# Performance work log

Measured on AMD Instinct MI355X. Metric: run time of the kernel, lower is better.

The kernel has to match this reference:

```python
import jax, jax.numpy as jnp
import numpy as np

U, I, NB = 200000, 100000, 50000
D = 64
NUM_LAYERS = 2
TEMP = 0.25      # conf['c_temps']
ALPHA = 0.5      # conf['alpha']
E_UI, E_UB, E_BI = 4_000_000, 2_000_000, 2_000_000
BT = 4096


def _segsum(vals, idx, gathered, n):
    # SpMM: out[idx] += vals * gathered   (COO sparse matmul)
    return jax.ops.segment_sum(vals[:, None] * gathered, idx, num_segments=n)


def _propagate(xa, xb, rows, cols, vals, layers):
    # LightGCN-style propagation over the symmetric bipartite block matrix
    # [[0, A], [A^T, 0]] with layer averaging.
    acc_a, acc_b = xa, xb
    for _ in range(layers):
        na = _segsum(vals, rows, xb[cols], xa.shape[0])
        nb = _segsum(vals, cols, xa[rows], xb.shape[0])
        xa, xb = na, nb
        acc_a = acc_a + xa
        acc_b = acc_b + xb
    inv = 1.0 / (layers + 1)
    return acc_a * inv, acc_b * inv


def _info_nce(a, b, temp):
    a = a * jax.lax.rsqrt(jnp.sum(a * a, -1, keepdims=True) + 1e-8)
    b = b * jax.lax.rsqrt(jnp.sum(b * b, -1, keepdims=True) + 1e-8)
    logits = (a @ b.T) / temp                      # [BT, BT]
    return jnp.mean(jax.nn.logsumexp(logits, axis=-1) - jnp.diagonal(logits))


def setup_inputs() -> dict:
    key = jax.random.key(0)
    ks = jax.random.split(key, 20)
    sc = 1.0 / np.sqrt(D)
    f32 = jnp.float32
    return {
        "users_feat": jax.random.normal(ks[0], (U, D), f32) * sc,
        "bundles_feat": jax.random.normal(ks[1], (NB, D), f32) * sc,
        "items_feat": jax.random.normal(ks[2], (I, D), f32) * sc,
        "L1_w": jax.random.normal(ks[3], (3, 3), f32) * 0.5,
        "L1_b": jnp.zeros((3,), f32),
        "L2_w": jax.random.normal(ks[4], (3, 3), f32) * 0.5,
        "L2_b": jnp.zeros((3,), f32),
        "L3_w": jax.random.normal(ks[5], (1, 3), f32) * 0.5,
        "L3_b": jnp.zeros((1,), f32),
        "ui_val": jax.random.uniform(ks[6], (E_UI,), f32, 0.0, 0.05),
        "ub_val": jax.random.uniform(ks[7], (E_UB,), f32, 0.0, 0.05),
        "bi_val": jax.random.uniform(ks[8], (E_BI,), f32, 0.0, 0.05),
        "ui_row": jax.random.randint(ks[9], (E_UI,), 0, U, jnp.int32),
        "ui_col": jax.random.randint(ks[10], (E_UI,), 0, I, jnp.int32),
        "ub_row": jax.random.randint(ks[11], (E_UB,), 0, U, jnp.int32),
        "ub_col": jax.random.randint(ks[12], (E_UB,), 0, NB, jnp.int32),
        "bi_row": jax.random.randint(ks[13], (E_BI,), 0, NB, jnp.int32),
        "bi_col": jax.random.randint(ks[14], (E_BI,), 0, I, jnp.int32),
        "users_idx": jax.random.randint(ks[15], (BT,), 0, U, jnp.int32),
        "bundles_idx": jax.random.randint(ks[16], (BT, 2), 0, NB, jnp.int32),
    }


def reference(users_feat, bundles_feat, items_feat, L1_w, L1_b, L2_w, L2_b,
              L3_w, L3_b, ui_val, ub_val, bi_val, ui_row, ui_col, ub_row,
              ub_col, bi_row, bi_col, users_idx, bundles_idx):
    # View 1: item-level main graph (u-i Laplacian propagation), bundle rep
    # aggregated from item embeddings via the row-normalized b-i graph.
    u1, i1 = _propagate(users_feat, items_feat, ui_row, ui_col, ui_val, NUM_LAYERS)
    b1 = _segsum(bi_val, bi_row, i1[bi_col], NB)
    # View 2: bundle-level main graph (u-b Laplacian propagation).
    u2, b2 = _propagate(users_feat, bundles_feat, ub_row, ub_col, ub_val, NUM_LAYERS)
    # View 3: sub views, one-hop row-normalized aggregation of raw item embs.
    u3 = _segsum(ui_val, ui_row, items_feat[ui_col], U)
    b3 = _segsum(bi_val, bi_row, items_feat[bi_col], NB)

    ue = jnp.stack([u1[users_idx], u2[users_idx], u3[users_idx]], axis=-1)      # [BT,D,3]
    be = jnp.stack([b1[bundles_idx], b2[bundles_idx], b3[bundles_idx]], axis=-1)  # [BT,2,D,3]
    s = jnp.einsum('bdv,bpdv->bpv', ue, be)                                      # [BT,2,3]

    # L1/L2/L3 view-fusion MLP (3 -> 3 -> 3 -> 1)
    h = jnp.tanh(s @ L1_w.T + L1_b)
    h = jnp.tanh(h @ L2_w.T + L2_b)
    pred = (h @ L3_w.T + L3_b)[..., 0]                                           # [BT,2]

    # BPR: -log sigmoid(pos - neg) == softplus(neg - pos)
    bpr = jnp.mean(jax.nn.softplus(-(pred[:, 0] - pred[:, 1])))
    cl = (_info_nce(u1[users_idx], u2[users_idx], TEMP)
          + _info_nce(b1[bundles_idx[:, 0]], b2[bundles_idx[:, 0]], TEMP))
    return bpr + ALPHA * cl
```

## Files before the change

### kernel.cpp

```cpp
#include <hip/hip_runtime.h>
#include <math.h>

#define DD 64
#define SCAN_TPB 256
#define SCAN_EPT 8
#define SCAN_EPB (SCAN_TPB * SCAN_EPT)
#define NCHUNK 8

__device__ __forceinline__ float bf2f(unsigned short u) {
    return __uint_as_float(((unsigned)u) << 16);
}
__device__ __forceinline__ unsigned short f2bf(float x) {
    unsigned b = __float_as_uint(x);
    unsigned r = (b + 0x7fffu + ((b >> 16) & 1u)) >> 16;
    return (unsigned short)r;
}


__global__ void hist_chunked_kernel(int* __restrict__ cnt, const int* __restrict__ tgt,
                                    int E, int n) {
    int myc = blockIdx.x & (NCHUNK - 1);
    int sub = blockIdx.x >> 3;
    int nsub = gridDim.x >> 3;
    int start = sub * blockDim.x + threadIdx.x;
    int stride = nsub * blockDim.x;
    for (int e = start; e < E; e += stride) {
        int t_ = tgt[e];
        int c = (int)(((long long)t_ * NCHUNK) / n);
        if (c == myc) atomicAdd(&cnt[t_], 1);
    }
}

__global__ void scatter_pairs_chunked(int2* __restrict__ pairs, int* __restrict__ cursor,
                                      const int* __restrict__ tgt, const int* __restrict__ src,
                                      const float* __restrict__ val, int E, int n) {
    int myc = blockIdx.x & (NCHUNK - 1);
    int sub = blockIdx.x >> 3;
    int nsub = gridDim.x >> 3;
    int start = sub * blockDim.x + threadIdx.x;
    int stride = nsub * blockDim.x;
    for (int e = start; e < E; e += stride) {
        int t_ = tgt[e];
        int c = (int)(((long long)t_ * NCHUNK) / n);
        if (c == myc) {
            int2 pr;
            pr.x = src[e];
            pr.y = __float_as_int(val[e]);
            int p = atomicAdd(&cursor[t_], 1);
            pairs[p] = pr;
        }
    }
}

__global__ void mark_kernel(int* __restrict__ mark, const int* __restrict__ idx, int n) {
    int g = blockIdx.x * blockDim.x + threadIdx.x;
    if (g < n) mark[idx[g]] = 1;
}

__global__ void hist_marked_kernel(int* __restrict__ cnt, const int* __restrict__ tgt,
                                   const int* __restrict__ mark, int E) {
    int g = blockIdx.x * blockDim.x + threadIdx.x;
    int stride = gridDim.x * blockDim.x;
    for (int e = g; e < E; e += stride) {
        int t_ = tgt[e];
        if (mark[t_]) atomicAdd(&cnt[t_], 1);
    }
}

__global__ void scatter_marked_kernel(int2* __restrict__ pairs, int* __restrict__ cursor,
                                      const int* __restrict__ tgt, const int* __restrict__ src,
                                      const float* __restrict__ val,
                                      const int* __restrict__ mark, int E) {
    int g = blockIdx.x * blockDim.x + threadIdx.x;
    int stride = gridDim.x * blockDim.x;
    for (int e = g; e < E; e += stride) {
        int t_ = tgt[e];
        if (mark[t_]) {
            int2 pr;
            pr.x = src[e];
            pr.y = __float_as_int(val[e]);
            int p = atomicAdd(&cursor[t_], 1);
            pairs[p] = pr;
        }
    }
}

__global__ void scan_pass1(int* __restrict__ blocksum, const int* __restrict__ cnt, int n) {
    int base = blockIdx.x * SCAN_EPB + threadIdx.x * SCAN_EPT;
    int s = 0;
#pragma unroll
    for (int k = 0; k < SCAN_EPT; ++k) {
        int i = base + k;
        if (i < n) s += cnt[i];
    }
#pragma unroll
    for (int o = 32; o >= 1; o >>= 1) s += __shfl_xor(s, o);
    __shared__ int ws_[4];
    if ((threadIdx.x & 63) == 0) ws_[threadIdx.x >> 6] = s;
    __syncthreads();
    if (threadIdx.x == 0) blocksum[blockIdx.x] = ws_[0] + ws_[1] + ws_[2] + ws_[3];
}

__global__ void scan_pass2(int* __restrict__ blocksum, int nb, int* __restrict__ ptr_n) {
    __shared__ int sh[1024];
    int t = threadIdx.x;
    int v = (t < nb) ? blocksum[t] : 0;
    sh[t] = v;
    __syncthreads();
    for (int o = 1; o < 1024; o <<= 1) {
        int x = (t >= o) ? sh[t - o] : 0;
        __syncthreads();
        sh[t] += x;
        __syncthreads();
    }
    if (t < nb) blocksum[t] = sh[t] - v;
    if (t == nb - 1) ptr_n[0] = sh[t];
}

__global__ void scan_pass3(int* __restrict__ ptr, int* __restrict__ cursor,
                           const int* __restrict__ cnt, const int* __restrict__ blockoff,
                           int n) {
    int base = blockIdx.x * SCAN_EPB + threadIdx.x * SCAN_EPT;
    int vals[SCAN_EPT];
    int s = 0;
#pragma unroll
    for (int k = 0; k < SCAN_EPT; ++k) {
        int i = base + k;
        int c = (i < n) ? cnt[i] : 0;
        vals[k] = s;
        s += c;
    }
    int incl = s;
#pragma unroll
    for (int o = 1; o < 64; o <<= 1) {
        int x = __shfl_up(incl, o);
        if ((threadIdx.x & 63) >= o) incl += x;
    }
    __shared__ int wtot[4];
    if ((threadIdx.x & 63) == 63) wtot[threadIdx.x >> 6] = incl;
    __syncthreads();
    int woff = 0;
    int wv = threadIdx.x >> 6;
    for (int k = 0; k < 4; ++k)
        if (k < wv) woff += wtot[k];
    int texcl = incl - s + woff + blockoff[blockIdx.x];
#pragma unroll
    for (int k = 0; k < SCAN_EPT; ++k) {
        int i = base + k;
        if (i < n) {
            int p = texcl + vals[k];
            ptr[i] = p;
            cursor[i] = p;
        }
    }
}

__global__ void spmm_kernel(const float* __restrict__ inf, const unsigned short* __restrict__ inb,
                            const int2* __restrict__ pairs, const int* __restrict__ ptr,
                            int nrows, const int* __restrict__ rowidx,
                            float* __restrict__ out, unsigned short* __restrict__ outb,
                            const float* __restrict__ add1,
                            const float* __restrict__ add2f,
                            const unsigned short* __restrict__ add2b,
                            float scale1,
                            const float* __restrict__ in2f, const unsigned short* __restrict__ in2b,
                            float* __restrict__ out2, const float* __restrict__ addB,
                            float f, float scale2) {
    int w = (int)(((unsigned)blockIdx.x * blockDim.x + threadIdx.x) >> 6);
    int lane = threadIdx.x & 63;
    if (w >= nrows) return;
    int r = rowidx ? rowidx[w] : w;
    int p = ptr[r];
    int end = ptr[r + 1];
    size_t outoff = (size_t)w * DD + lane;
    size_t nodeoff = (size_t)r * DD + lane;
    float acc = 0.f, acc2 = 0.f;
    const bool dual = (in2f != nullptr) || (in2b != nullptr);
    for (; p + 8 <= end; p += 8) {
        int ss[8];
        float vv[8];
#pragma unroll
        for (int k = 0; k < 8; ++k) {
            int2 pr = pairs[p + k];
            ss[k] = __builtin_amdgcn_readfirstlane(pr.x);
            vv[k] = __int_as_float(__builtin_amdgcn_readfirstlane(pr.y));
        }
        if (inb) {
#pragma unroll
            for (int k = 0; k < 8; ++k) acc += vv[k] * bf2f(inb[(size_t)ss[k] * DD + lane]);
        } else {
#pragma unroll
            for (int k = 0; k < 8; ++k) acc += vv[k] * inf[(size_t)ss[k] * DD + lane];
        }
        if (dual) {
            if (in2b) {
#pragma unroll
                for (int k = 0; k < 8; ++k) acc2 += vv[k] * bf2f(in2b[(size_t)ss[k] * DD + lane]);
            } else {
#pragma unroll
                for (int k = 0; k < 8; ++k) acc2 += vv[k] * in2f[(size_t)ss[k] * DD + lane];
            }
        }
    }
    for (; p < end; ++p) {
        int2 pr = pairs[p];
        int s = __builtin_amdgcn_readfirstlane(pr.x);
        float v = __int_as_float(__builtin_amdgcn_readfirstlane(pr.y));
        acc += v * (inb ? bf2f(inb[(size_t)s * DD + lane]) : inf[(size_t)s * DD + lane]);
        if (dual)
            acc2 += v * (in2b ? bf2f(in2b[(size_t)s * DD + lane]) : in2f[(size_t)s * DD + lane]);
    }
    float rr = acc;
    if (add1) rr += add1[nodeoff];
    if (add2f) rr += add2f[nodeoff];
    if (add2b) rr += bf2f(add2b[nodeoff]);
    rr *= scale1;
    if (out) out[outoff] = rr;
    if (outb) outb[outoff] = f2bf(rr);
    if (dual) {
        float r2 = acc2 + f * acc;
        if (addB) r2 += addB[nodeoff];
        out2[outoff] = r2 * scale2;
    }
}


__global__ void f2bf_kernel(unsigned short* __restrict__ o, const float* __restrict__ i,
                            long long n4) {
    long long g = (long long)blockIdx.x * blockDim.x + threadIdx.x;
    long long stride = (long long)gridDim.x * blockDim.x;
    for (long long t = g; t < n4; t += stride) {
        float4 v = ((const float4*)i)[t];
        ushort4 u;
        u.x = f2bf(v.x); u.y = f2bf(v.y); u.z = f2bf(v.z); u.w = f2bf(v.w);
        ((ushort4*)o)[t] = u;
    }
}

__global__ void gather_rows_bf16_kernel(float* __restrict__ raw,
                                        const unsigned short* __restrict__ src,
                                        const int* __restrict__ idx, int nrows) {
    int g = blockIdx.x * blockDim.x + threadIdx.x;
    if (g >= nrows * DD) return;
    int r = g >> 6;
    raw[g] = bf2f(src[(size_t)idx[r] * DD + (g & 63)]);
}

__global__ void norm_rows_kernel(float* __restrict__ nrm, const float* __restrict__ src,
                                 int nrows, int rstride) {
    int r = blockIdx.x;
    if (r >= nrows) return;
    int d = threadIdx.x;
    float v = src[(size_t)r * rstride * DD + d];
    float ss = v * v;
#pragma unroll
    for (int o = 32; o >= 1; o >>= 1) ss += __shfl_xor(ss, o);
    nrm[(size_t)r * DD + d] = v * rsqrtf(ss + 1e-8f);
}

__global__ void transpose64_kernel(float* __restrict__ out, const float* __restrict__ in,
                                   int n) {
    __shared__ float T[64][65];
    int b0 = blockIdx.x * 64;
    int t = threadIdx.x;
#pragma unroll
    for (int k = 0; k < 4; ++k) {
        int f = k * 1024 + t * 4;
        int r = f >> 6, c = f & 63;
        float4 v = *(const float4*)(in + (size_t)(b0 + r) * 64 + c);
        T[r][c] = v.x; T[r][c + 1] = v.y; T[r][c + 2] = v.z; T[r][c + 3] = v.w;
    }
    __syncthreads();
#pragma unroll
    for (int k = 0; k < 4; ++k) {
        int f = k * 1024 + t * 4;
        int d = f >> 6, c = f & 63;
        float4 v;
        v.x = T[c][d]; v.y = T[c + 1][d]; v.z = T[c + 2][d]; v.w = T[c + 3][d];
        *(float4*)(out + (size_t)d * n + b0 + c) = v;
    }
}

__global__ void batch_pred_kernel(const float* __restrict__ u1b, const float* __restrict__ u2b,
                                  const float* __restrict__ u3b,
                                  const float* __restrict__ b1b, const float* __restrict__ b2b,
                                  const float* __restrict__ b3b,
                                  const float* __restrict__ W1, const float* __restrict__ c1,
                                  const float* __restrict__ W2, const float* __restrict__ c2,
                                  const float* __restrict__ W3, const float* __restrict__ c3,
                                  float* __restrict__ acc, int nb) {
    int b = blockIdx.x;
    if (b >= nb) return;
    int d = threadIdx.x;
    float ud1 = u1b[(size_t)b * DD + d];
    float ud2 = u2b[(size_t)b * DD + d];
    float ud3 = u3b[(size_t)b * DD + d];
    float pred[2];
#pragma unroll
    for (int p = 0; p < 2; ++p) {
        size_t r = (size_t)(b * 2 + p) * DD + d;
        float s0 = ud1 * b1b[r];
        float s1 = ud2 * b2b[r];
        float s2 = ud3 * b3b[r];
#pragma unroll
        for (int o = 32; o >= 1; o >>= 1) {
            s0 += __shfl_xor(s0, o);
            s1 += __shfl_xor(s1, o);
            s2 += __shfl_xor(s2, o);
        }
        float t0 = tanhf(s0 * W1[0] + s1 * W1[1] + s2 * W1[2] + c1[0]);
        float t1 = tanhf(s0 * W1[3] + s1 * W1[4] + s2 * W1[5] + c1[1]);
        float t2 = tanhf(s0 * W1[6] + s1 * W1[7] + s2 * W1[8] + c1[2]);
        float g0 = tanhf(t0 * W2[0] + t1 * W2[1] + t2 * W2[2] + c2[0]);
        float g1 = tanhf(t0 * W2[3] + t1 * W2[4] + t2 * W2[5] + c2[1]);
        float g2 = tanhf(t0 * W2[6] + t1 * W2[7] + t2 * W2[8] + c2[2]);
        pred[p] = g0 * W3[0] + g1 * W3[1] + g2 * W3[2] + c3[0];
    }
    if (d == 0) {
        float x = pred[1] - pred[0];
        float sp = (x > 20.0f) ? x : log1pf(expf(x));
        unsafeAtomicAdd(acc, sp);
    }
}

__global__ void nce_part_kernel(const float* __restrict__ A, const float* __restrict__ Bt,
                                float* __restrict__ pm, float* __restrict__ ps,
                                float* __restrict__ pd, int n, float invtemp) {
    int wv = threadIdx.x >> 6;
    int lane = threadIdx.x & 63;
    int row = blockIdx.x;
    float4 a4[16];
    const float4* Ap = (const float4*)(A + (size_t)row * DD);
#pragma unroll
    for (int q = 0; q < 16; ++q) a4[q] = Ap[q];
    int quarter = n >> 2;
    int c0 = wv * quarter;
    float m = -1e30f, ssum = 0.0f, diag = 0.0f;
    int ntile = quarter >> 8;
    for (int t = 0; t < ntile; ++t) {
        int j0 = c0 + (t << 8) + (lane << 2);
        float dx = 0.f, dy = 0.f, dz = 0.f, dw = 0.f;
#pragma unroll
        for (int q = 0; q < 16; ++q) {
            float4 a = a4[q];
            float4 r0 = *(const float4*)(Bt + (size_t)(4 * q + 0) * n + j0);
            float4 r1 = *(const float4*)(Bt + (size_t)(4 * q + 1) * n + j0);
            float4 r2 = *(const float4*)(Bt + (size_t)(4 * q + 2) * n + j0);
            float4 r3 = *(const float4*)(Bt + (size_t)(4 * q + 3) * n + j0);
            dx += a.x * r0.x + a.y * r1.x + a.z * r2.x + a.w * r3.x;
            dy += a.x * r0.y + a.y * r1.y + a.z * r2.y + a.w * r3.y;
            dz += a.x * r0.z + a.y * r1.z + a.z * r2.z + a.w * r3.z;
            dw += a.x * r0.w + a.y * r1.w + a.z * r2.w + a.w * r3.w;
        }
        float lg[4] = {dx * invtemp, dy * invtemp, dz * invtemp, dw * invtemp};
#pragma unroll
        for (int k = 0; k < 4; ++k) {
            if (j0 + k == row) diag = lg[k];
            float mn = fmaxf(m, lg[k]);
            ssum = ssum * __expf(m - mn) + __expf(lg[k] - mn);
            m = mn;
        }
    }
#pragma unroll
    for (int o = 32; o >= 1; o >>= 1) {
        float m2 = __shfl_xor(m, o);
        float s2 = __shfl_xor(ssum, o);
        float d2 = __shfl_xor(diag, o);
        float mn = fmaxf(m, m2);
        ssum = ssum * __expf(m - mn) + s2 * __expf(m2 - mn);
        m = mn;
        diag += d2;
    }
    if (lane == 0) {
        pm[row * 4 + wv] = m;
        ps[row * 4 + wv] = ssum;
        pd[row * 4 + wv] = diag;
    }
}

__global__ void nce_merge_kernel(const float* __restrict__ pm, const float* __restrict__ ps,
                                 const float* __restrict__ pd, float* __restrict__ acc,
                                 int nrows) {
    int r = blockIdx.x * blockDim.x + threadIdx.x;
    float v = 0.0f;
    if (r < nrows) {
        float m = -1e30f, s = 0.f, d = 0.f;
#pragma unroll
        for (int q = 0; q < 4; ++q) {
            float mq = pm[r * 4 + q], sq = ps[r * 4 + q];
            d += pd[r * 4 + q];
            float mn = fmaxf(m, mq);
            s = s * __expf(m - mn) + sq * __expf(mq - mn);
            m = mn;
        }
        v = m + logf(s) - d;
    }
#pragma unroll
    for (int o = 32; o >= 1; o >>= 1) v += __shfl_xor(v, o);
    if ((threadIdx.x & 63) == 0) unsafeAtomicAdd(acc, v);
}

__global__ void final_kernel(const float* __restrict__ acc, float* __restrict__ out,
                             float invn, float alpha) {
    out[0] = acc[0] * invn + alpha * invn * (acc[1] + acc[2]);
}


extern "C" void kernel_launch(void* const* d_in, const int* in_sizes, int n_in,
                              void* d_out, int out_size, void* d_ws, size_t ws_size,
                              hipStream_t stream) {
    const float* users_feat   = (const float*)d_in[0];
    const float* bundles_feat = (const float*)d_in[1];
    const float* items_feat   = (const float*)d_in[2];
    const float* W1 = (const float*)d_in[3];
    const float* c1 = (const float*)d_in[4];
    const float* W2 = (const float*)d_in[5];
    const float* c2 = (const float*)d_in[6];
    const float* W3 = (const float*)d_in[7];
    const float* c3 = (const float*)d_in[8];
    const float* ui_val = (const float*)d_in[9];
    const float* ub_val = (const float*)d_in[10];
    const float* bi_val = (const float*)d_in[11];
    const int* ui_row = (const int*)d_in[12];
    const int* ui_col = (const int*)d_in[13];
    const int* ub_row = (const int*)d_in[14];
    const int* ub_col = (const int*)d_in[15];
    const int* bi_row = (const int*)d_in[16];
    const int* bi_col = (const int*)d_in[17];
    const int* uidx = (const int*)d_in[18];
    const int* bidx = (const int*)d_in[19];

    const int U  = in_sizes[0] / DD;
    const int NB = in_sizes[1] / DD;
    const int I  = in_sizes[2] / DD;
    const int Eui = in_sizes[9];
    const int Eub = in_sizes[10];
    const int Ebi = in_sizes[11];
    const int BT = in_sizes[18];

    const size_t U64  = (size_t)U * DD;
    const size_t I64  = (size_t)I * DD;
    const size_t NB64 = (size_t)NB * DD;
    const size_t BT64 = (size_t)BT * DD;

    float* w = (float*)d_ws;
    size_t o = 0;
    float* RA  = w + o; o += I64;
    float* RB  = w + o; o += I64;
    float* u3b = w + o; o += BT64;
    float* u1b = w + o; o += BT64;
    float* u2b = w + o; o += BT64;
    float* b1b = w + o; o += 2 * BT64;
    float* b2b = w + o; o += 2 * BT64;
    float* b3b = w + o; o += 2 * BT64;
    float* A1  = w + o; o += BT64;
    float* A2  = w + o; o += BT64;
    float* B1n = w + o; o += BT64;
    float* B2n = w + o; o += BT64;
    float* pm  = w + o; o += (size_t)BT * 4;
    float* ps  = w + o; o += (size_t)BT * 4;
    float* pd  = w + o; o += (size_t)BT * 4;
    float* acc = w + o; o += 16;

    unsigned short* Ubf = (unsigned short*)(w + o); o += (U64 + 1) / 2;
    unsigned short* Ibf = (unsigned short*)(w + o); o += (I64 + 1) / 2;
    unsigned short* Bbf = (unsigned short*)(w + o); o += (NB64 + 1) / 2;
    unsigned short* Xbf = (unsigned short*)(w + o); o += (U64 + 1) / 2;

    int nmax = U; if (I > nmax) nmax = I; if (NB > nmax) nmax = NB;
    int emax = Eui; if (Eub > emax) emax = Eub; if (Ebi > emax) emax = Ebi;
    int* ib = (int*)(w + o);
    size_t io_ = 0;
    int* cnt  = ib + io_; io_ += (size_t)nmax + 1;
    int* bsum = ib + io_; io_ += 1025;
    int* mark = ib + io_; io_ += (size_t)NB + 1;
    int* ptrA = ib + io_; io_ += (size_t)nmax + 1;
    int* ptrB = ib + io_; io_ += (size_t)nmax + 1;
    io_ = (io_ + 3) & ~(size_t)3;
    int2* pairsA = (int2*)(ib + io_); io_ += (size_t)emax * 2;
    int2* pairsB = (int2*)(ib + io_); io_ += (size_t)emax * 2;

    float* A2t = (float*)pairsA;
    float* B2t = A2t + BT64;

    auto build = [&](int2* pairs, int* ptr_, const int* tgt, const int* src,
                     const float* val, int n, int E) {
        hipMemsetAsync(cnt, 0, ((size_t)n + 1) * sizeof(int), stream);
        hist_chunked_kernel<<<8192, 256, 0, stream>>>(cnt, tgt, E, n);
        int nb_ = (n + SCAN_EPB - 1) / SCAN_EPB;
        scan_pass1<<<nb_, SCAN_TPB, 0, stream>>>(bsum, cnt, n);
        scan_pass2<<<1, 1024, 0, stream>>>(bsum, nb_, ptr_ + n);
        scan_pass3<<<nb_, SCAN_TPB, 0, stream>>>(ptr_, cnt, cnt, bsum, n);
        scatter_pairs_chunked<<<8192, 256, 0, stream>>>(pairs, cnt, tgt, src, val, E, n);
    };
    auto spmm = [&](const float* inf, const unsigned short* inb,
                    const int2* pairs, const int* ptr_, int nrows, const int* rowidx,
                    float* out, unsigned short* outb,
                    const float* add1, const float* add2f, const unsigned short* add2b,
                    float scale1,
                    const float* in2f, const unsigned short* in2b,
                    float* out2, const float* addB, float f, float scale2) {
        int blocks = (nrows + 3) / 4;
        spmm_kernel<<<blocks, 256, 0, stream>>>(inf, inb, pairs, ptr_, nrows, rowidx,
                                                out, outb, add1, add2f, add2b, scale1,
                                                in2f, in2b, out2, addB, f, scale2);
    };
    const float k3 = 1.0f / 3.0f;
    const float* NF = nullptr;
    const unsigned short* NB16 = nullptr;
    const int* NI = nullptr;

    f2bf_kernel<<<2048, 256, 0, stream>>>(Ubf, users_feat, (long long)(U64 / 4));
    f2bf_kernel<<<1024, 256, 0, stream>>>(Ibf, items_feat, (long long)(I64 / 4));
    f2bf_kernel<<<512, 256, 0, stream>>>(Bbf, bundles_feat, (long long)(NB64 / 4));

    build(pairsA, ptrA, ui_row, ui_col, ui_val, U, Eui);
    spmm(NF, Ibf, pairsA, ptrA, U, NI,
         nullptr, Xbf, NF, NF, NB16, 1.f, NF, NB16, nullptr, NF, 0.f, 1.f);
    gather_rows_bf16_kernel<<<(BT * DD + 255) / 256, 256, 0, stream>>>(u3b, Xbf, uidx, BT);
    build(pairsB, ptrB, ui_col, ui_row, ui_val, I, Eui);
    spmm(NF, Ubf, pairsB, ptrB, I, NI,
         RA, nullptr, NF, NF, NB16, 1.f,
         NF, Xbf, RB, items_feat, 1.f, k3);
    spmm(RA, NB16, pairsA, ptrA, BT, uidx,
         u1b, nullptr, users_feat, NF, Xbf, k3, NF, NB16, nullptr, NF, 0.f, 1.f);
    norm_rows_kernel<<<BT, 64, 0, stream>>>(A1, u1b, BT, 1);

    hipMemsetAsync(mark, 0, ((size_t)NB + 1) * sizeof(int), stream);
    mark_kernel<<<(2 * BT + 255) / 256, 256, 0, stream>>>(mark, bidx, 2 * BT);
    hipMemsetAsync(cnt, 0, ((size_t)NB + 1) * sizeof(int), stream);
    {
        int gb = (Ebi + 255) / 256; if (gb > 4096) gb = 4096;
        hist_marked_kernel<<<gb, 256, 0, stream>>>(cnt, bi_row, mark, Ebi);
        int nb_ = (NB + SCAN_EPB - 1) / SCAN_EPB;
        scan_pass1<<<nb_, SCAN_TPB, 0, stream>>>(bsum, cnt, NB);
        scan_pass2<<<1, 1024, 0, stream>>>(bsum, nb_, ptrA + NB);
        scan_pass3<<<nb_, SCAN_TPB, 0, stream>>>(ptrA, cnt, cnt, bsum, NB);
        scatter_marked_kernel<<<gb, 256, 0, stream>>>(pairsA, cnt, bi_row, bi_col,
                                                      bi_val, mark, Ebi);
    }
    spmm(RB, NB16, pairsA, ptrA, 2 * BT, bidx,
         b1b, nullptr, NF, NF, NB16, 1.f,
         NF, Ibf, b3b, NF, 0.f, 1.f);
    norm_rows_kernel<<<BT, 64, 0, stream>>>(B1n, b1b, BT, 2);

    build(pairsA, ptrA, ub_row, ub_col, ub_val, U, Eub);
    spmm(NF, Bbf, pairsA, ptrA, U, NI,
         nullptr, Xbf, NF, NF, NB16, 1.f, NF, NB16, nullptr, NF, 0.f, 1.f);
    build(pairsB, ptrB, ub_col, ub_row, ub_val, NB, Eub);
    spmm(NF, Ubf, pairsB, ptrB, NB, NI,
         RA, nullptr, NF, NF, NB16, 1.f, NF, NB16, nullptr, NF, 0.f, 1.f);
    spmm(RA, NB16, pairsA, ptrA, BT, uidx,
         u2b, nullptr, users_feat, NF, Xbf, k3, NF, NB16, nullptr, NF, 0.f, 1.f);
    norm_rows_kernel<<<BT, 64, 0, stream>>>(A2, u2b, BT, 1);
    spmm(NF, Xbf, pairsB, ptrB, 2 * BT, bidx,
         b2b, nullptr, bundles_feat, RA, NB16, k3, NF, NB16, nullptr, NF, 0.f, 1.f);
    norm_rows_kernel<<<BT, 64, 0, stream>>>(B2n, b2b, BT, 2);

    transpose64_kernel<<<BT / 64, 256, 0, stream>>>(A2t, A2, BT);
    transpose64_kernel<<<BT / 64, 256, 0, stream>>>(B2t, B2n, BT);

    hipMemsetAsync(acc, 0, 4 * sizeof(float), stream);

    batch_pred_kernel<<<BT, 64, 0, stream>>>(u1b, u2b, u3b, b1b, b2b, b3b,
                                             W1, c1, W2, c2, W3, c3, acc, BT);

    nce_part_kernel<<<BT, 256, 0, stream>>>(A1, A2t, pm, ps, pd, BT, 4.0f);
    nce_merge_kernel<<<(BT + 255) / 256, 256, 0, stream>>>(pm, ps, pd, acc + 1, BT);
    nce_part_kernel<<<BT, 256, 0, stream>>>(B1n, B2t, pm, ps, pd, BT, 4.0f);
    nce_merge_kernel<<<(BT + 255) / 256, 256, 0, stream>>>(pm, ps, pd, acc + 2, BT);

    final_kernel<<<1, 1, 0, stream>>>(acc, (float*)d_out, 1.0f / (float)BT, 0.5f);
}
```

Measured before the change: 2.330 ms.

## Compute InfoNCE logits with bf16 MFMA and fuse row normalization into SpMM

Replaces the scalar fp32 InfoNCE dot-product kernel, its merge kernel and the transposes with one MFMA-based kernel. It takes bf16 normalized rows and handles both contrastive terms in a single launch, doing the online logsumexp per 16-row tile. Row L2 normalization moves into the SpMM epilogue, which writes bf16 directly and removes the separate normalize kernels. The cost is bf16 precision in the logits. The InfoNCE stage is only a small part of a runtime dominated by the sparse builds and SpMMs.

```diff
diff --git a/kernel.cpp b/kernel.cpp
--- a/kernel.cpp
+++ b/kernel.cpp
@@ -6,6 +6,9 @@
 #define SCAN_EPT 8
 #define SCAN_EPB (SCAN_TPB * SCAN_EPT)
 #define NCHUNK 8
+
+typedef short bf16x8 __attribute__((ext_vector_type(8)));
+typedef float f32x4 __attribute__((ext_vector_type(4)));
 
 __device__ __forceinline__ float bf2f(unsigned short u) {
     return __uint_as_float(((unsigned)u) << 16);
@@ -165,7 +168,8 @@
                             float scale1,
                             const float* __restrict__ in2f, const unsigned short* __restrict__ in2b,
                             float* __restrict__ out2, const float* __restrict__ addB,
-                            float f, float scale2) {
+                            float f, float scale2,
+                            unsigned short* __restrict__ nrmOut, int nrmEvery) {
     int w = (int)(((unsigned)blockIdx.x * blockDim.x + threadIdx.x) >> 6);
     int lane = threadIdx.x & 63;
     if (w >= nrows) return;
@@ -222,6 +226,12 @@
         if (addB) r2 += addB[nodeoff];
         out2[outoff] = r2 * scale2;
     }
+    if (nrmOut && (nrmEvery == 1 || (w & 1) == 0)) {
+        float sq = rr * rr;
+#pragma unroll
+        for (int o = 32; o >= 1; o >>= 1) sq += __shfl_xor(sq, o);
+        nrmOut[(size_t)(w / nrmEvery) * DD + lane] = f2bf(rr * rsqrtf(sq + 1e-8f));
+    }
 }
 
 
@@ -244,41 +254,6 @@
     if (g >= nrows * DD) return;
     int r = g >> 6;
     raw[g] = bf2f(src[(size_t)idx[r] * DD + (g & 63)]);
-}
-
-__global__ void norm_rows_kernel(float* __restrict__ nrm, const float* __restrict__ src,
-                                 int nrows, int rstride) {
-    int r = blockIdx.x;
-    if (r >= nrows) return;
-    int d = threadIdx.x;
-    float v = src[(size_t)r * rstride * DD + d];
-    float ss = v * v;
-#pragma unroll
-    for (int o = 32; o >= 1; o >>= 1) ss += __shfl_xor(ss, o);
-    nrm[(size_t)r * DD + d] = v * rsqrtf(ss + 1e-8f);
-}
-
-__global__ void transpose64_kernel(float* __restrict__ out, const float* __restrict__ in,
-                                   int n) {
-    __shared__ float T[64][65];
-    int b0 = blockIdx.x * 64;
-    int t = threadIdx.x;
-#pragma unroll
-    for (int k = 0; k < 4; ++k) {
-        int f = k * 1024 + t * 4;
-        int r = f >> 6, c = f & 63;
-        float4 v = *(const float4*)(in + (size_t)(b0 + r) * 64 + c);
-        T[r][c] = v.x; T[r][c + 1] = v.y; T[r][c + 2] = v.z; T[r][c + 3] = v.w;
-    }
-    __syncthreads();
-#pragma unroll
-    for (int k = 0; k < 4; ++k) {
-        int f = k * 1024 + t * 4;
-        int d = f >> 6, c = f & 63;
-        float4 v;
-        v.x = T[c][d]; v.y = T[c + 1][d]; v.z = T[c + 2][d]; v.w = T[c + 3][d];
-        *(float4*)(out + (size_t)d * n + b0 + c) = v;
-    }
 }
 
 __global__ void batch_pred_kernel(const float* __restrict__ u1b, const float* __restrict__ u2b,
@@ -323,81 +298,91 @@
     }
 }
 
-__global__ void nce_part_kernel(const float* __restrict__ A, const float* __restrict__ Bt,
-                                float* __restrict__ pm, float* __restrict__ ps,
-                                float* __restrict__ pd, int n, float invtemp) {
-    int wv = threadIdx.x >> 6;
-    int lane = threadIdx.x & 63;
-    int row = blockIdx.x;
-    float4 a4[16];
-    const float4* Ap = (const float4*)(A + (size_t)row * DD);
-#pragma unroll
-    for (int q = 0; q < 16; ++q) a4[q] = Ap[q];
-    int quarter = n >> 2;
-    int c0 = wv * quarter;
-    float m = -1e30f, ssum = 0.0f, diag = 0.0f;
-    int ntile = quarter >> 8;
+__global__ void nce_mfma_kernel(const unsigned short* __restrict__ A1,
+                                const unsigned short* __restrict__ B1, float* __restrict__ acc1,
+                                const unsigned short* __restrict__ A2,
+                                const unsigned short* __restrict__ B2, float* __restrict__ acc2,
+                                int n, float invtemp) {
+    int nbv = n >> 4;
+    const unsigned short* A;
+    const unsigned short* B;
+    float* accp;
+    int blk = blockIdx.x;
+    if (blk < nbv) { A = A1; B = B1; accp = acc1; }
+    else           { blk -= nbv; A = A2; B = B2; accp = acc2; }
+    int row0 = blk << 4;
+    int wv = threadIdx.x >> 6, lane = threadIdx.x & 63;
+    int li = lane & 15, lq = lane >> 4;
+
+    const bf16x8* Ap = (const bf16x8*)(A + (size_t)(row0 + li) * DD + lq * 8);
+    bf16x8 af0 = Ap[0];
+    bf16x8 af1 = Ap[4];
+
+    int qcols = n >> 2;
+    int c0 = wv * qcols;
+    int ntile = qcols >> 4;
+    float m[4] = {-1e30f, -1e30f, -1e30f, -1e30f};
+    float sm[4] = {0.f, 0.f, 0.f, 0.f};
+    float dg[4] = {0.f, 0.f, 0.f, 0.f};
     for (int t = 0; t < ntile; ++t) {
-        int j0 = c0 + (t << 8) + (lane << 2);
-        float dx = 0.f, dy = 0.f, dz = 0.f, dw = 0.f;
-#pragma unroll
-        for (int q = 0; q < 16; ++q) {
-            float4 a = a4[q];
-            float4 r0 = *(const float4*)(Bt + (size_t)(4 * q + 0) * n + j0);
-            float4 r1 = *(const float4*)(Bt + (size_t)(4 * q + 1) * n + j0);
-            float4 r2 = *(const float4*)(Bt + (size_t)(4 * q + 2) * n + j0);
-            float4 r3 = *(const float4*)(Bt + (size_t)(4 * q + 3) * n + j0);
-            dx += a.x * r0.x + a.y * r1.x + a.z * r2.x + a.w * r3.x;
-            dy += a.x * r0.y + a.y * r1.y + a.z * r2.y + a.w * r3.y;
-            dz += a.x * r0.z + a.y * r1.z + a.z * r2.z + a.w * r3.z;
-            dw += a.x * r0.w + a.y * r1.w + a.z * r2.w + a.w * r3.w;
-        }
-        float lg[4] = {dx * invtemp, dy * invtemp, dz * invtemp, dw * invtemp};
-#pragma unroll
-        for (int k = 0; k < 4; ++k) {
-            if (j0 + k == row) diag = lg[k];
-            float mn = fmaxf(m, lg[k]);
-            ssum = ssum * __expf(m - mn) + __expf(lg[k] - mn);
-            m = mn;
-        }
-    }
-#pragma unroll
-    for (int o = 32; o >= 1; o >>= 1) {
-        float m2 = __shfl_xor(m, o);
-        float s2 = __shfl_xor(ssum, o);
-        float d2 = __shfl_xor(diag, o);
-        float mn = fmaxf(m, m2);
-        ssum = ssum * __expf(m - mn) + s2 * __expf(m2 - mn);
-        m = mn;
-        diag += d2;
-    }
-    if (lane == 0) {
-        pm[row * 4 + wv] = m;
-        ps[row * 4 + wv] = ssum;
-        pd[row * 4 + wv] = diag;
-    }
-}
-
-__global__ void nce_merge_kernel(const float* __restrict__ pm, const float* __restrict__ ps,
-                                 const float* __restrict__ pd, float* __restrict__ acc,
-                                 int nrows) {
-    int r = blockIdx.x * blockDim.x + threadIdx.x;
-    float v = 0.0f;
-    if (r < nrows) {
-        float m = -1e30f, s = 0.f, d = 0.f;
+        int colbase = c0 + (t << 4);
+        const bf16x8* Bp = (const bf16x8*)(B + (size_t)(colbase + li) * DD + lq * 8);
+        bf16x8 bf0 = Bp[0];
+        bf16x8 bf1 = Bp[4];
+        f32x4 z = {0.f, 0.f, 0.f, 0.f};
+        f32x4 s = __builtin_amdgcn_mfma_f32_16x16x32_bf16(af0, bf0, z, 0, 0, 0);
+        s = __builtin_amdgcn_mfma_f32_16x16x32_bf16(af1, bf1, s, 0, 0, 0);
+        int col = colbase + li;
+#pragma unroll
+        for (int r = 0; r < 4; ++r) {
+            float l = s[r] * invtemp;
+            int row = row0 + (lq << 2) + r;
+            if (col == row) dg[r] = l;
+            float mn = fmaxf(m[r], l);
+            sm[r] = sm[r] * __expf(m[r] - mn) + __expf(l - mn);
+            m[r] = mn;
+        }
+    }
+#pragma unroll
+    for (int r = 0; r < 4; ++r) {
+        float mm = m[r], ss = sm[r], dd = dg[r];
+#pragma unroll
+        for (int o = 1; o <= 8; o <<= 1) {
+            float m2 = __shfl_xor(mm, o);
+            float s2 = __shfl_xor(ss, o);
+            float d2 = __shfl_xor(dd, o);
+            float mn = fmaxf(mm, m2);
+            ss = ss * __expf(mm - mn) + s2 * __expf(m2 - mn);
+            mm = mn;
+            dd += d2;
+        }
+        m[r] = mm; sm[r] = ss; dg[r] = dd;
+    }
+    __shared__ float pM[4][16], pS[4][16], pD[4][16];
+    if (li == 0) {
+#pragma unroll
+        for (int r = 0; r < 4; ++r) {
+            pM[wv][(lq << 2) + r] = m[r];
+            pS[wv][(lq << 2) + r] = sm[r];
+            pD[wv][(lq << 2) + r] = dg[r];
+        }
+    }
+    __syncthreads();
+    if (wv == 0 && lane < 16) {
+        float mm = -1e30f, ss = 0.f, dd = 0.f;
 #pragma unroll
         for (int q = 0; q < 4; ++q) {
-            float mq = pm[r * 4 + q], sq = ps[r * 4 + q];
-            d += pd[r * 4 + q];
-            float mn = fmaxf(m, mq);
-            s = s * __expf(m - mn) + sq * __expf(mq - mn);
-            m = mn;
-        }
-        v = m + logf(s) - d;
-    }
-#pragma unroll
-    for (int o = 32; o >= 1; o >>= 1) v += __shfl_xor(v, o);
-    if ((threadIdx.x & 63) == 0) unsafeAtomicAdd(acc, v);
+            float mq = pM[q][lane], sq = pS[q][lane];
+            dd += pD[q][lane];
+            float mn = fmaxf(mm, mq);
+            ss = ss * __expf(mm - mn) + sq * __expf(mq - mn);
+            mm = mn;
+        }
+        float v = mm + logf(ss) - dd;
+#pragma unroll
+        for (int o = 1; o <= 8; o <<= 1) v += __shfl_xor(v, o);
+        if (lane == 0) unsafeAtomicAdd(accp, v);
+    }
 }
 
 __global__ void final_kernel(const float* __restrict__ acc, float* __restrict__ out,
@@ -453,13 +438,10 @@
     float* b1b = w + o; o += 2 * BT64;
     float* b2b = w + o; o += 2 * BT64;
     float* b3b = w + o; o += 2 * BT64;
-    float* A1  = w + o; o += BT64;
-    float* A2  = w + o; o += BT64;
-    float* B1n = w + o; o += BT64;
-    float* B2n = w + o; o += BT64;
-    float* pm  = w + o; o += (size_t)BT * 4;
-    float* ps  = w + o; o += (size_t)BT * 4;
-    float* pd  = w + o; o += (size_t)BT * 4;
+    unsigned short* A1  = (unsigned short*)(w + o); o += BT64 / 2;
+    unsigned short* A2  = (unsigned short*)(w + o); o += BT64 / 2;
+    unsigned short* B1n = (unsigned short*)(w + o); o += BT64 / 2;
+    unsigned short* B2n = (unsigned short*)(w + o); o += BT64 / 2;
     float* acc = w + o; o += 16;
 
     unsigned short* Ubf = (unsigned short*)(w + o); o += (U64 + 1) / 2;
@@ -479,9 +461,6 @@
     io_ = (io_ + 3) & ~(size_t)3;
     int2* pairsA = (int2*)(ib + io_); io_ += (size_t)emax * 2;
     int2* pairsB = (int2*)(ib + io_); io_ += (size_t)emax * 2;
-
-    float* A2t = (float*)pairsA;
-    float* B2t = A2t + BT64;
 
     auto build = [&](int2* pairs, int* ptr_, const int* tgt, const int* src,
                      const float* val, int n, int E) {
@@ -499,11 +478,13 @@
                     const float* add1, const float* add2f, const unsigned short* add2b,
                     float scale1,
                     const float* in2f, const unsigned short* in2b,
-                    float* out2, const float* addB, float f, float scale2) {
+                    float* out2, const float* addB, float f, float scale2,
+                    unsigned short* nrmOut, int nrmEvery) {
         int blocks = (nrows + 3) / 4;
         spmm_kernel<<<blocks, 256, 0, stream>>>(inf, inb, pairs, ptr_, nrows, rowidx,
                                                 out, outb, add1, add2f, add2b, scale1,
-                                                in2f, in2b, out2, addB, f, scale2);
+                                                in2f, in2b, out2, addB, f, scale2,
+                                                nrmOut, nrmEvery);
     };
     const float k3 = 1.0f / 3.0f;
     const float* NF = nullptr;
@@ -516,16 +497,17 @@
 
     build(pairsA, ptrA, ui_row, ui_col, ui_val, U, Eui);
     spmm(NF, Ibf, pairsA, ptrA, U, NI,
-         nullptr, Xbf, NF, NF, NB16, 1.f, NF, NB16, nullptr, NF, 0.f, 1.f);
+         nullptr, Xbf, NF, NF, NB16, 1.f, NF, NB16, nullptr, NF, 0.f, 1.f,
+         nullptr, 1);
     gather_rows_bf16_kernel<<<(BT * DD + 255) / 256, 256, 0, stream>>>(u3b, Xbf, uidx, BT);
     build(pairsB, ptrB, ui_col, ui_row, ui_val, I, Eui);
     spmm(NF, Ubf, pairsB, ptrB, I, NI,
          RA, nullptr, NF, NF, NB16, 1.f,
-         NF, Xbf, RB, items_feat, 1.f, k3);
+         NF, Xbf, RB, items_feat, 1.f, k3,
+         nullptr, 1);
     spmm(RA, NB16, pairsA, ptrA, BT, uidx,
-         u1b, nullptr, users_feat, NF, Xbf, k3, NF, NB16, nullptr, NF, 0.f, 1.f);
-    norm_rows_kernel<<<BT, 64, 0, stream>>>(A1, u1b, BT, 1);
-
+         u1b, nullptr, users_feat, NF, Xbf, k3, NF, NB16, nullptr, NF, 0.f, 1.f,
+         A1, 1);
     hipMemsetAsync(mark, 0, ((size_t)NB + 1) * sizeof(int), stream);
     mark_kernel<<<(2 * BT + 255) / 256, 256, 0, stream>>>(mark, bidx, 2 * BT);
     hipMemsetAsync(cnt, 0, ((size_t)NB + 1) * sizeof(int), stream);
@@ -541,34 +523,31 @@
     }
     spmm(RB, NB16, pairsA, ptrA, 2 * BT, bidx,
          b1b, nullptr, NF, NF, NB16, 1.f,
-         NF, Ibf, b3b, NF, 0.f, 1.f);
-    norm_rows_kernel<<<BT, 64, 0, stream>>>(B1n, b1b, BT, 2);
+         NF, Ibf, b3b, NF, 0.f, 1.f,
+         B1n, 2);
 
     build(pairsA, ptrA, ub_row, ub_col, ub_val, U, Eub);
     spmm(NF, Bbf, pairsA, ptrA, U, NI,
-         nullptr, Xbf, NF, NF, NB16, 1.f, NF, NB16, nullptr, NF, 0.f, 1.f);
+         nullptr, Xbf, NF, NF, NB16, 1.f, NF, NB16, nullptr, NF, 0.f, 1.f,
+         nullptr, 1);
     build(pairsB, ptrB, ub_col, ub_row, ub_val, NB, Eub);
     spmm(NF, Ubf, pairsB, ptrB, NB, NI,
-         RA, nullptr, NF, NF, NB16, 1.f, NF, NB16, nullptr, NF, 0.f, 1.f);
+         RA, nullptr, NF, NF, NB16, 1.f, NF, NB16, nullptr, NF, 0.f, 1.f,
+         nullptr, 1);
     spmm(RA, NB16, pairsA, ptrA, BT, uidx,
-         u2b, nullptr, users_feat, NF, Xbf, k3, NF, NB16, nullptr, NF, 0.f, 1.f);
-    norm_rows_kernel<<<BT, 64, 0, stream>>>(A2, u2b, BT, 1);
+         u2b, nullptr, users_feat, NF, Xbf, k3, NF, NB16, nullptr, NF, 0.f, 1.f,
+         A2, 1);
     spmm(NF, Xbf, pairsB, ptrB, 2 * BT, bidx,
-         b2b, nullptr, bundles_feat, RA, NB16, k3, NF, NB16, nullptr, NF, 0.f, 1.f);
-    norm_rows_kernel<<<BT, 64, 0, stream>>>(B2n, b2b, BT, 2);
-
-    transpose64_kernel<<<BT / 64, 256, 0, stream>>>(A2t, A2, BT);
-    transpose64_kernel<<<BT / 64, 256, 0, stream>>>(B2t, B2n, BT);
+         b2b, nullptr, bundles_feat, RA, NB16, k3, NF, NB16, nullptr, NF, 0.f, 1.f,
+         B2n, 2);
 
     hipMemsetAsync(acc, 0, 4 * sizeof(float), stream);
 
     batch_pred_kernel<<<BT, 64, 0, stream>>>(u1b, u2b, u3b, b1b, b2b, b3b,
                                              W1, c1, W2, c2, W3, c3, acc, BT);
 
-    nce_part_kernel<<<BT, 256, 0, stream>>>(A1, A2t, pm, ps, pd, BT, 4.0f);
-    nce_merge_kernel<<<(BT + 255) / 256, 256, 0, stream>>>(pm, ps, pd, acc + 1, BT);
-    nce_part_kernel<<<BT, 256, 0, stream>>>(B1n, B2t, pm, ps, pd, BT, 4.0f);
-    nce_merge_kernel<<<(BT + 255) / 256, 256, 0, stream>>>(pm, ps, pd, acc + 2, BT);
+    nce_mfma_kernel<<<2 * (BT / 16), 256, 0, stream>>>(A1, A2, acc + 1,
+                                                       B1n, B2n, acc + 2, BT, 4.0f);
 
     final_kernel<<<1, 1, 0, stream>>>(acc, (float*)d_out, 1.0f / (float)BT, 0.5f);
 }
```

Measured after the change: 2.005 ms. -13.9%, faster.
